# Optimization experiments

Hardware: AMD Instinct MI355X
Metric: run time of the kernel (lower is better)

## Reference

```python
import jax, jax.numpy as jnp
import numpy as np

B, T, F = 8192, 30, 16
H1, H2 = 64, 32


def _lstm(x, Wih, Whh, b):
    """PyTorch-convention LSTM (gate order i,f,g,o). x: [B,T,I] -> (ys [B,T,H], hT [B,H])."""
    H = Whh.shape[1]
    h0 = jnp.zeros((x.shape[0], H), x.dtype)

    def step(carry, xt):
        h, c = carry
        z = xt @ Wih.T + h @ Whh.T + b  # [B,4H]
        i, f, g, o = jnp.split(z, 4, axis=-1)
        c = jax.nn.sigmoid(f) * c + jax.nn.sigmoid(i) * jnp.tanh(g)
        h = jax.nn.sigmoid(o) * jnp.tanh(c)
        return (h, c), h

    (hT, _), ys = jax.lax.scan(step, (h0, h0), jnp.swapaxes(x, 0, 1))
    return jnp.swapaxes(ys, 0, 1), hT


def setup_inputs() -> dict:
    key = jax.random.key(0)
    ks = jax.random.split(key, 16)
    s = 0.1  # small init scale for numerical sanity
    return {
        "x": jax.random.normal(ks[0], (B, T, F), jnp.float32),
        "Wih1": jax.random.normal(ks[1], (4 * H1, F), jnp.float32) * s,
        "Whh1": jax.random.normal(ks[2], (4 * H1, H1), jnp.float32) * s,
        "b1": jax.random.normal(ks[3], (4 * H1,), jnp.float32) * s,
        "Wih2": jax.random.normal(ks[4], (4 * H2, H1), jnp.float32) * s,
        "Whh2": jax.random.normal(ks[5], (4 * H2, H2), jnp.float32) * s,
        "b2": jax.random.normal(ks[6], (4 * H2,), jnp.float32) * s,
        "Wih3": jax.random.normal(ks[7], (4 * H2, H2), jnp.float32) * s,
        "Whh3": jax.random.normal(ks[8], (4 * H2, H2), jnp.float32) * s,
        "b3": jax.random.normal(ks[9], (4 * H2,), jnp.float32) * s,
        "Wih4": jax.random.normal(ks[10], (4 * H1, H2), jnp.float32) * s,
        "Whh4": jax.random.normal(ks[11], (4 * H1, H1), jnp.float32) * s,
        "b4": jax.random.normal(ks[12], (4 * H1,), jnp.float32) * s,
        "Wout": jax.random.normal(ks[13], (F, H1), jnp.float32) * s,
        "bout": jax.random.normal(ks[14], (F,), jnp.float32) * s,
    }


def reference(x, Wih1, Whh1, b1, Wih2, Whh2, b2, Wih3, Whh3, b3, Wih4, Whh4, b4, Wout, bout):
    ys1, _ = _lstm(x, Wih1, Whh1, b1)          # encoder LSTM(64)
    _, latent = _lstm(ys1, Wih2, Whh2, b2)      # encoder LSTM(32) -> final hidden [B,32]
    repeated = jnp.broadcast_to(latent[:, None, :], (latent.shape[0], T, latent.shape[1]))
    ys3, _ = _lstm(repeated, Wih3, Whh3, b3)    # decoder LSTM(32)
    ys4, _ = _lstm(ys3, Wih4, Whh4, b4)         # decoder LSTM(64)
    return ys4 @ Wout.T + bout                  # [B,T,F]
```

## Files before the change

### kernel.cpp

```cpp
#include <hip/hip_runtime.h>


#define TT 30
#define FF 16

typedef unsigned short u16t;
typedef __attribute__((ext_vector_type(8))) short short8;
typedef __attribute__((ext_vector_type(4))) short short4v;
typedef __attribute__((ext_vector_type(4))) float floatx4;

#define MFMA(a, b, c) __builtin_amdgcn_mfma_f32_16x16x32_bf16(a, b, c, 0, 0, 0)

__device__ __forceinline__ float rcpf(float v) { return __builtin_amdgcn_rcpf(v); }
__device__ __forceinline__ float sigf(float v) { return rcpf(1.f + __expf(-v)); }
__device__ __forceinline__ float tanhf_(float v) { return 1.f - 2.f * rcpf(1.f + __expf(2.f * v)); }
__device__ __forceinline__ u16t f2bf(float f) {
  unsigned int u = __float_as_uint(f);
  u = (u + 0x7FFFu + ((u >> 16) & 1u)) >> 16;
  return (u16t)u;
}
__device__ __forceinline__ short8 ldFrag(const float* p) {
  const float4 lo = *(const float4*)p;
  const float4 hi = *(const float4*)(p + 4);
  short8 r;
  r[0] = (short)f2bf(lo.x); r[1] = (short)f2bf(lo.y);
  r[2] = (short)f2bf(lo.z); r[3] = (short)f2bf(lo.w);
  r[4] = (short)f2bf(hi.x); r[5] = (short)f2bf(hi.y);
  r[6] = (short)f2bf(hi.z); r[7] = (short)f2bf(hi.w);
  return r;
}
__device__ __forceinline__ float cellUp(const floatx4 acc, float& c) {
  float iv = sigf(acc[0]), fv = sigf(acc[1]);
  float gv = tanhf_(acc[2]), ov = sigf(acc[3]);
  c = fv * c + iv * gv;
  return ov * tanhf_(c);
}

__global__ __launch_bounds__(512, 4) void lstm_ae_mfma2(
    const float* __restrict__ x,
    const float* __restrict__ Wih1, const float* __restrict__ Whh1, const float* __restrict__ b1,
    const float* __restrict__ Wih2, const float* __restrict__ Whh2, const float* __restrict__ b2,
    const float* __restrict__ Wih3, const float* __restrict__ Whh3, const float* __restrict__ b3,
    const float* __restrict__ Wih4, const float* __restrict__ Whh4, const float* __restrict__ b4,
    const float* __restrict__ Wout, const float* __restrict__ bout,
    float* __restrict__ out)
{
  __shared__ __align__(16) u16t big[16 * 1992];
  __shared__ __align__(16) u16t aB[16 * 200];

  const int t = threadIdx.x;
  const int w = t >> 6, lane = t & 63;
  const int q = lane >> 4, n = lane & 15;
  const int q8 = q * 8, n200 = n * 200;
  const int n968 = n * 968, n1992 = n * 1992;
  const int bBase = blockIdx.x * 16;
  const int nlo = n >> 2, ngt = n & 3;

  for (int i = t; i < 16 * 200; i += 512) aB[i] = 0;
  {
    const float* xb = x + (size_t)bBase * (TT * FF);
    for (int i4 = t; i4 < 1920; i4 += 512) {
      int e = i4 * 4;
      int b = e / 480, r = e - b * 480;
      int stp = r >> 4, f = r & 15;
      float4 v = *(const float4*)&xb[e];
      short4v s4 = { (short)f2bf(v.x), (short)f2bf(v.y), (short)f2bf(v.z), (short)f2bf(v.w) };
      *(short4v*)&big[b * 968 + stp * 32 + f] = s4;
    }
    for (int i = t; i < 7680; i += 512) {
      int b = i / 480, r = i - b * 480;
      int stp = r >> 4, f = r & 15;
      big[b * 968 + stp * 32 + 16 + f] = 0;
    }
  }
  short8 w1f[2][3]; floatx4 bias1[2];
  const short8 z8 = { 0, 0, 0, 0, 0, 0, 0, 0 };
#pragma unroll
  for (int tt = 0; tt < 2; ++tt) {
    int row = ngt * 64 + (2 * w + tt) * 4 + nlo;
    w1f[tt][0] = z8;
    if (q < 2) w1f[tt][0] = ldFrag(&Wih1[row * 16 + q8]);
    w1f[tt][1] = ldFrag(&Whh1[row * 64 + q8]);
    w1f[tt][2] = ldFrag(&Whh1[row * 64 + 32 + q8]);
#pragma unroll
    for (int r = 0; r < 4; ++r) bias1[tt][r] = b1[r * 64 + (2 * w + tt) * 4 + q];
  }
  short8 w2f[3]; floatx4 bias2;
  {
    int row = ngt * 32 + w * 4 + nlo;
    w2f[0] = ldFrag(&Wih2[row * 64 + q8]);
    w2f[1] = ldFrag(&Wih2[row * 64 + 32 + q8]);
    w2f[2] = ldFrag(&Whh2[row * 32 + q8]);
#pragma unroll
    for (int r = 0; r < 4; ++r) bias2[r] = b2[r * 32 + w * 4 + q];
  }
  __syncthreads();

  float c1v[2] = {0.f, 0.f}, c2v = 0.f;

  for (int st = 0; st < TT; ++st) {
    const int p = st & 1;
    const int h1o = 32 + p * 64, h1n = 32 + (1 - p) * 64;
    const int h2o = p ? 160 : 0, h2n = p ? 0 : 160;
    const short8 bx   = *(const short8*)&big[n968 + st * 32 + q8];
    const short8 bh1a = *(const short8*)&aB[n200 + h1o + q8];
    const short8 bh1b = *(const short8*)&aB[n200 + h1o + 32 + q8];
    const short8 bh2  = *(const short8*)&aB[n200 + h2o + q8];
    floatx4 a0 = bias1[0], a1 = bias1[1];
    a0 = MFMA(w1f[0][0], bx, a0);   a1 = MFMA(w1f[1][0], bx, a1);
    a0 = MFMA(w1f[0][1], bh1a, a0); a1 = MFMA(w1f[1][1], bh1a, a1);
    a0 = MFMA(w1f[0][2], bh1b, a0); a1 = MFMA(w1f[1][2], bh1b, a1);
    aB[n200 + h1n + (2 * w) * 4 + q]     = f2bf(cellUp(a0, c1v[0]));
    aB[n200 + h1n + (2 * w + 1) * 4 + q] = f2bf(cellUp(a1, c1v[1]));
    __syncthreads();
    const short8 bh1na = *(const short8*)&aB[n200 + h1n + q8];
    const short8 bh1nb = *(const short8*)&aB[n200 + h1n + 32 + q8];
    floatx4 a2 = bias2;
    a2 = MFMA(w2f[0], bh1na, a2);
    a2 = MFMA(w2f[1], bh1nb, a2);
    a2 = MFMA(w2f[2], bh2, a2);
    aB[n200 + h2n + w * 4 + q] = f2bf(cellUp(a2, c2v));
    __syncthreads();
  }

  const short8 blat = *(const short8*)&aB[n200 + q8];
  short8 w3f[2]; floatx4 bias3;
  {
    int row = ngt * 32 + w * 4 + nlo;
    w3f[0] = ldFrag(&Wih3[row * 32 + q8]);
    w3f[1] = ldFrag(&Whh3[row * 32 + q8]);
#pragma unroll
    for (int r = 0; r < 4; ++r) bias3[r] = b3[r * 32 + w * 4 + q];
  }
  short8 w4f[2][3]; floatx4 bias4[2];
#pragma unroll
  for (int tt = 0; tt < 2; ++tt) {
    int row = ngt * 64 + (2 * w + tt) * 4 + nlo;
    w4f[tt][0] = ldFrag(&Wih4[row * 32 + q8]);
    w4f[tt][1] = ldFrag(&Whh4[row * 64 + q8]);
    w4f[tt][2] = ldFrag(&Whh4[row * 64 + 32 + q8]);
#pragma unroll
    for (int r = 0; r < 4; ++r) bias4[tt][r] = b4[r * 64 + (2 * w + tt) * 4 + q];
  }
  short8 wof[2];
  wof[0] = ldFrag(&Wout[n * 64 + q8]);
  wof[1] = ldFrag(&Wout[n * 64 + 32 + q8]);
  const floatx4 biasO = *(const floatx4*)&bout[q * 4];
  for (int i = t; i < 1024; i += 512) aB[(i >> 6) * 200 + 64 + (i & 63)] = 0;
  for (int i = t; i < 1024; i += 512) big[(i >> 6) * 1992 + (i & 63)] = 0;
  __syncthreads();

  float c3v = 0.f, c4v[2] = {0.f, 0.f};

  for (int st = 0; st < TT; ++st) {
    const int p = st & 1;
    const int h3o = 64 + p * 32, h3n = 64 + (1 - p) * 32;
    const short8 bh3  = *(const short8*)&aB[n200 + h3o + q8];
    const short8 bh4a = *(const short8*)&big[n1992 + st * 64 + q8];
    const short8 bh4b = *(const short8*)&big[n1992 + st * 64 + 32 + q8];
    floatx4 a3 = bias3;
    a3 = MFMA(w3f[0], blat, a3);
    a3 = MFMA(w3f[1], bh3, a3);
    aB[n200 + h3n + w * 4 + q] = f2bf(cellUp(a3, c3v));
    __syncthreads();
    const short8 bh3n = *(const short8*)&aB[n200 + h3n + q8];
    floatx4 a40 = bias4[0], a41 = bias4[1];
    a40 = MFMA(w4f[0][0], bh3n, a40); a41 = MFMA(w4f[1][0], bh3n, a41);
    a40 = MFMA(w4f[0][1], bh4a, a40); a41 = MFMA(w4f[1][1], bh4a, a41);
    a40 = MFMA(w4f[0][2], bh4b, a40); a41 = MFMA(w4f[1][2], bh4b, a41);
    big[n1992 + (st + 1) * 64 + (2 * w) * 4 + q]     = f2bf(cellUp(a40, c4v[0]));
    big[n1992 + (st + 1) * 64 + (2 * w + 1) * 4 + q] = f2bf(cellUp(a41, c4v[1]));
    __syncthreads();
  }

  for (int s = w * 4; s < w * 4 + 4 && s < TT; ++s) {
    const short8 ba = *(const short8*)&big[n1992 + (s + 1) * 64 + q8];
    const short8 bb = *(const short8*)&big[n1992 + (s + 1) * 64 + 32 + q8];
    floatx4 yv = biasO;
    yv = MFMA(wof[0], ba, yv);
    yv = MFMA(wof[1], bb, yv);
    *(floatx4*)&out[((size_t)(bBase + n) * TT + s) * FF + q * 4] = yv;
  }
}

extern "C" void kernel_launch(void* const* d_in, const int* in_sizes, int n_in,
                              void* d_out, int out_size, void* d_ws, size_t ws_size,
                              hipStream_t stream) {
  const float* x    = (const float*)d_in[0];
  const float* Wih1 = (const float*)d_in[1];
  const float* Whh1 = (const float*)d_in[2];
  const float* b1   = (const float*)d_in[3];
  const float* Wih2 = (const float*)d_in[4];
  const float* Whh2 = (const float*)d_in[5];
  const float* b2   = (const float*)d_in[6];
  const float* Wih3 = (const float*)d_in[7];
  const float* Whh3 = (const float*)d_in[8];
  const float* b3   = (const float*)d_in[9];
  const float* Wih4 = (const float*)d_in[10];
  const float* Whh4 = (const float*)d_in[11];
  const float* b4   = (const float*)d_in[12];
  const float* Wout = (const float*)d_in[13];
  const float* bout = (const float*)d_in[14];
  float* out = (float*)d_out;

  const int B = in_sizes[0] / (TT * FF);
  dim3 grid(B / 16), block(512);
  lstm_ae_mfma2<<<grid, block, 0, stream>>>(
      x, Wih1, Whh1, b1, Wih2, Whh2, b2, Wih3, Whh3, b3,
      Wih4, Whh4, b4, Wout, bout, out);
}
```

Measured before the change: 172.4 us.

## Wavefront-skew stacked LSTM layers to halve per-step barriers and fuse output projection

Skews the two encoder layers and the two decoder layers by one timestep so layer 2 at step t and layer 1 at step t+1 run in the same iteration, needing one __syncthreads per step instead of two. The decoder's output projection is folded into the recurrent loop, with one wave per step computing it, so the large per-timestep h4 history buffer is no longer kept. Shared memory drops from roughly 70KB to about 39KB, which could allow more resident blocks. The cost is prologue/epilogue code and more live registers per iteration.

```diff
diff --git a/kernel.cpp b/kernel.cpp
--- a/kernel.cpp
+++ b/kernel.cpp
@@ -36,7 +36,7 @@
   return ov * tanhf_(c);
 }
 
-__global__ __launch_bounds__(512, 4) void lstm_ae_mfma2(
+__global__ __launch_bounds__(512, 4) void lstm_ae_mfma3(
     const float* __restrict__ x,
     const float* __restrict__ Wih1, const float* __restrict__ Whh1, const float* __restrict__ b1,
     const float* __restrict__ Wih2, const float* __restrict__ Whh2, const float* __restrict__ b2,
@@ -45,18 +45,18 @@
     const float* __restrict__ Wout, const float* __restrict__ bout,
     float* __restrict__ out)
 {
-  __shared__ __align__(16) u16t big[16 * 1992];
-  __shared__ __align__(16) u16t aB[16 * 200];
+  __shared__ __align__(16) u16t xAll[16 * 968];
+  __shared__ __align__(16) u16t aB[16 * 264];
 
   const int t = threadIdx.x;
   const int w = t >> 6, lane = t & 63;
   const int q = lane >> 4, n = lane & 15;
-  const int q8 = q * 8, n200 = n * 200;
-  const int n968 = n * 968, n1992 = n * 1992;
+  const int q8 = q * 8, n264 = n * 264, n968 = n * 968;
   const int bBase = blockIdx.x * 16;
   const int nlo = n >> 2, ngt = n & 3;
-
-  for (int i = t; i < 16 * 200; i += 512) aB[i] = 0;
+  const u16t* aRow = &aB[n264];
+
+  for (int i = t; i < 16 * 264; i += 512) aB[i] = 0;
   {
     const float* xb = x + (size_t)bBase * (TT * FF);
     for (int i4 = t; i4 < 1920; i4 += 512) {
@@ -65,12 +65,12 @@
       int stp = r >> 4, f = r & 15;
       float4 v = *(const float4*)&xb[e];
       short4v s4 = { (short)f2bf(v.x), (short)f2bf(v.y), (short)f2bf(v.z), (short)f2bf(v.w) };
-      *(short4v*)&big[b * 968 + stp * 32 + f] = s4;
+      *(short4v*)&xAll[b * 968 + stp * 32 + f] = s4;
     }
     for (int i = t; i < 7680; i += 512) {
       int b = i / 480, r = i - b * 480;
       int stp = r >> 4, f = r & 15;
-      big[b * 968 + stp * 32 + 16 + f] = 0;
+      xAll[b * 968 + stp * 32 + 16 + f] = 0;
     }
   }
   short8 w1f[2][3]; floatx4 bias1[2];
@@ -98,32 +98,46 @@
 
   float c1v[2] = {0.f, 0.f}, c2v = 0.f;
 
-  for (int st = 0; st < TT; ++st) {
+  {
+    const short8 bx = *(const short8*)&xAll[n968 + q8];
+    floatx4 a0 = bias1[0], a1 = bias1[1];
+    a0 = MFMA(w1f[0][0], bx, a0); a1 = MFMA(w1f[1][0], bx, a1);
+    aB[n264 + (2 * w) * 4 + q]     = f2bf(cellUp(a0, c1v[0]));
+    aB[n264 + (2 * w + 1) * 4 + q] = f2bf(cellUp(a1, c1v[1]));
+  }
+  __syncthreads();
+
+  for (int st = 0; st < TT - 1; ++st) {
     const int p = st & 1;
-    const int h1o = 32 + p * 64, h1n = 32 + (1 - p) * 64;
-    const int h2o = p ? 160 : 0, h2n = p ? 0 : 160;
-    const short8 bx   = *(const short8*)&big[n968 + st * 32 + q8];
-    const short8 bh1a = *(const short8*)&aB[n200 + h1o + q8];
-    const short8 bh1b = *(const short8*)&aB[n200 + h1o + 32 + q8];
-    const short8 bh2  = *(const short8*)&aB[n200 + h2o + q8];
+    const short8 bh1a = *(const short8*)&aRow[p * 64 + q8];
+    const short8 bh1b = *(const short8*)&aRow[p * 64 + 32 + q8];
+    const short8 bh2  = *(const short8*)&aRow[128 + (1 - p) * 32 + q8];
+    const short8 bx   = *(const short8*)&xAll[n968 + (st + 1) * 32 + q8];
+    floatx4 a2 = bias2;
+    a2 = MFMA(w2f[0], bh1a, a2);
+    a2 = MFMA(w2f[1], bh1b, a2);
+    a2 = MFMA(w2f[2], bh2, a2);
     floatx4 a0 = bias1[0], a1 = bias1[1];
     a0 = MFMA(w1f[0][0], bx, a0);   a1 = MFMA(w1f[1][0], bx, a1);
     a0 = MFMA(w1f[0][1], bh1a, a0); a1 = MFMA(w1f[1][1], bh1a, a1);
     a0 = MFMA(w1f[0][2], bh1b, a0); a1 = MFMA(w1f[1][2], bh1b, a1);
-    aB[n200 + h1n + (2 * w) * 4 + q]     = f2bf(cellUp(a0, c1v[0]));
-    aB[n200 + h1n + (2 * w + 1) * 4 + q] = f2bf(cellUp(a1, c1v[1]));
+    aB[n264 + 128 + p * 32 + w * 4 + q]        = f2bf(cellUp(a2, c2v));
+    aB[n264 + (1 - p) * 64 + (2 * w) * 4 + q]  = f2bf(cellUp(a0, c1v[0]));
+    aB[n264 + (1 - p) * 64 + (2 * w + 1) * 4 + q] = f2bf(cellUp(a1, c1v[1]));
     __syncthreads();
-    const short8 bh1na = *(const short8*)&aB[n200 + h1n + q8];
-    const short8 bh1nb = *(const short8*)&aB[n200 + h1n + 32 + q8];
+  }
+  {
+    const short8 bh1a = *(const short8*)&aRow[64 + q8];
+    const short8 bh1b = *(const short8*)&aRow[96 + q8];
+    const short8 bh2  = *(const short8*)&aRow[128 + q8];
     floatx4 a2 = bias2;
-    a2 = MFMA(w2f[0], bh1na, a2);
-    a2 = MFMA(w2f[1], bh1nb, a2);
+    a2 = MFMA(w2f[0], bh1a, a2);
+    a2 = MFMA(w2f[1], bh1b, a2);
     a2 = MFMA(w2f[2], bh2, a2);
-    aB[n200 + h2n + w * 4 + q] = f2bf(cellUp(a2, c2v));
-    __syncthreads();
-  }
-
-  const short8 blat = *(const short8*)&aB[n200 + q8];
+    aB[n264 + 160 + w * 4 + q] = f2bf(cellUp(a2, c2v));
+  }
+  __syncthreads();
+
   short8 w3f[2]; floatx4 bias3;
   {
     int row = ngt * 32 + w * 4 + nlo;
@@ -146,40 +160,67 @@
   wof[0] = ldFrag(&Wout[n * 64 + q8]);
   wof[1] = ldFrag(&Wout[n * 64 + 32 + q8]);
   const floatx4 biasO = *(const floatx4*)&bout[q * 4];
-  for (int i = t; i < 1024; i += 512) aB[(i >> 6) * 200 + 64 + (i & 63)] = 0;
-  for (int i = t; i < 1024; i += 512) big[(i >> 6) * 1992 + (i & 63)] = 0;
+  const short8 blat = *(const short8*)&aRow[160 + q8];
+  for (int i = t; i < 1024; i += 512) aB[(i >> 6) * 264 + 64 + (i & 63)] = 0;
   __syncthreads();
 
   float c3v = 0.f, c4v[2] = {0.f, 0.f};
 
-  for (int st = 0; st < TT; ++st) {
+  {
+    floatx4 a3 = bias3;
+    a3 = MFMA(w3f[0], blat, a3);
+    aB[n264 + 192 + w * 4 + q] = f2bf(cellUp(a3, c3v));
+  }
+  __syncthreads();
+
+  for (int st = 0; st < TT - 1; ++st) {
     const int p = st & 1;
-    const int h3o = 64 + p * 32, h3n = 64 + (1 - p) * 32;
-    const short8 bh3  = *(const short8*)&aB[n200 + h3o + q8];
-    const short8 bh4a = *(const short8*)&big[n1992 + st * 64 + q8];
-    const short8 bh4b = *(const short8*)&big[n1992 + st * 64 + 32 + q8];
+    const short8 bh3  = *(const short8*)&aRow[192 + p * 32 + q8];
+    const short8 bh4a = *(const short8*)&aRow[(1 - p) * 64 + q8];
+    const short8 bh4b = *(const short8*)&aRow[(1 - p) * 64 + 32 + q8];
+    floatx4 a40 = bias4[0], a41 = bias4[1];
+    a40 = MFMA(w4f[0][0], bh3, a40);  a41 = MFMA(w4f[1][0], bh3, a41);
+    a40 = MFMA(w4f[0][1], bh4a, a40); a41 = MFMA(w4f[1][1], bh4a, a41);
+    a40 = MFMA(w4f[0][2], bh4b, a40); a41 = MFMA(w4f[1][2], bh4b, a41);
     floatx4 a3 = bias3;
     a3 = MFMA(w3f[0], blat, a3);
     a3 = MFMA(w3f[1], bh3, a3);
-    aB[n200 + h3n + w * 4 + q] = f2bf(cellUp(a3, c3v));
+    aB[n264 + p * 64 + (2 * w) * 4 + q]     = f2bf(cellUp(a40, c4v[0]));
+    aB[n264 + p * 64 + (2 * w + 1) * 4 + q] = f2bf(cellUp(a41, c4v[1]));
+    aB[n264 + 192 + (1 - p) * 32 + w * 4 + q] = f2bf(cellUp(a3, c3v));
+    if (st > 0 && w == ((st - 1) & 7)) {
+      floatx4 yv = biasO;
+      yv = MFMA(wof[0], bh4a, yv);
+      yv = MFMA(wof[1], bh4b, yv);
+      *(floatx4*)&out[((size_t)(bBase + n) * TT + (st - 1)) * FF + q * 4] = yv;
+    }
     __syncthreads();
-    const short8 bh3n = *(const short8*)&aB[n200 + h3n + q8];
+  }
+  {
+    const short8 bh3  = *(const short8*)&aRow[224 + q8];
+    const short8 bh4a = *(const short8*)&aRow[q8];
+    const short8 bh4b = *(const short8*)&aRow[32 + q8];
     floatx4 a40 = bias4[0], a41 = bias4[1];
-    a40 = MFMA(w4f[0][0], bh3n, a40); a41 = MFMA(w4f[1][0], bh3n, a41);
+    a40 = MFMA(w4f[0][0], bh3, a40);  a41 = MFMA(w4f[1][0], bh3, a41);
     a40 = MFMA(w4f[0][1], bh4a, a40); a41 = MFMA(w4f[1][1], bh4a, a41);
     a40 = MFMA(w4f[0][2], bh4b, a40); a41 = MFMA(w4f[1][2], bh4b, a41);
-    big[n1992 + (st + 1) * 64 + (2 * w) * 4 + q]     = f2bf(cellUp(a40, c4v[0]));
-    big[n1992 + (st + 1) * 64 + (2 * w + 1) * 4 + q] = f2bf(cellUp(a41, c4v[1]));
-    __syncthreads();
-  }
-
-  for (int s = w * 4; s < w * 4 + 4 && s < TT; ++s) {
-    const short8 ba = *(const short8*)&big[n1992 + (s + 1) * 64 + q8];
-    const short8 bb = *(const short8*)&big[n1992 + (s + 1) * 64 + 32 + q8];
+    aB[n264 + 64 + (2 * w) * 4 + q]     = f2bf(cellUp(a40, c4v[0]));
+    aB[n264 + 64 + (2 * w + 1) * 4 + q] = f2bf(cellUp(a41, c4v[1]));
+    if (w == 4) {
+      floatx4 yv = biasO;
+      yv = MFMA(wof[0], bh4a, yv);
+      yv = MFMA(wof[1], bh4b, yv);
+      *(floatx4*)&out[((size_t)(bBase + n) * TT + 28) * FF + q * 4] = yv;
+    }
+  }
+  __syncthreads();
+  if (w == 5) {
+    const short8 ba = *(const short8*)&aRow[64 + q8];
+    const short8 bb = *(const short8*)&aRow[96 + q8];
     floatx4 yv = biasO;
     yv = MFMA(wof[0], ba, yv);
     yv = MFMA(wof[1], bb, yv);
-    *(floatx4*)&out[((size_t)(bBase + n) * TT + s) * FF + q * 4] = yv;
+    *(floatx4*)&out[((size_t)(bBase + n) * TT + 29) * FF + q * 4] = yv;
   }
 }
 
@@ -205,7 +246,7 @@
 
   const int B = in_sizes[0] / (TT * FF);
   dim3 grid(B / 16), block(512);
-  lstm_ae_mfma2<<<grid, block, 0, stream>>>(
+  lstm_ae_mfma3<<<grid, block, 0, stream>>>(
       x, Wih1, Whh1, b1, Wih2, Whh2, b2, Wih3, Whh3, b3,
       Wih4, Whh4, b4, Wout, bout, out);
 }
```

New measurement: 171.7 us. No clear change (-0.4%).
